# Kernel tuning notes

Measured on AMD Instinct MI355X. Metric: run time of the kernel, lower is better.

## Reference

```python
import jax, jax.numpy as jnp
import numpy as np

N = 100000   # nodes
E = 3200000  # edges (avg degree 32)
F = 128      # num_features
H = 256      # hidden_dim
D = 256      # embedding_dim
O = 2        # output_dim
BN_EPS = 1e-5


def _mk_layer(keys, fin, fmid, fout):
    kW1, kW2 = keys
    W1 = jax.random.normal(kW1, (fin, fmid), jnp.float32) / np.sqrt(fin)
    b1 = jnp.zeros((fmid,), jnp.float32)
    g = jnp.ones((fmid,), jnp.float32)
    be = jnp.zeros((fmid,), jnp.float32)
    mu = jnp.zeros((fmid,), jnp.float32)
    var = jnp.ones((fmid,), jnp.float32)
    W2 = jax.random.normal(kW2, (fmid, fout), jnp.float32) / np.sqrt(fmid)
    b2 = jnp.zeros((fout,), jnp.float32)
    return W1, b1, g, be, mu, var, W2, b2


def setup_inputs() -> dict:
    key = jax.random.key(0)
    ks = jax.random.split(key, 10)
    inp = {}
    inp["x"] = jax.random.normal(ks[0], (N, F), jnp.float32)
    inp["edge_index"] = jax.random.randint(ks[1], (2, E), 0, N, jnp.int32)
    names = ["W1", "b1", "g", "be", "mu", "var", "W2", "b2"]
    for pref, (fin, fmid, fout), kk in [
        ("l1", (F, H, H), (ks[2], ks[3])),
        ("l2", (H, H, H), (ks[4], ks[5])),
        ("l3", (H, H, D), (ks[6], ks[7])),
    ]:
        vals = _mk_layer(kk, fin, fmid, fout)
        for n, v in zip(names, vals):
            inp[f"{pref}_{n}"] = v
    inp["out_W"] = jax.random.normal(ks[8], (D, O), jnp.float32) / np.sqrt(D)
    inp["out_b"] = jnp.zeros((O,), jnp.float32)
    return inp


def gin_layer(h, src, dst, W1, b1, g, be, mu, var, W2, b2, final_relu):
    # GINConv (eps=0): z_i = x_i + sum_{j->i} x_j, then MLP(Linear-BN-ReLU-Linear[-ReLU])
    agg = jax.ops.segment_sum(h[src], dst, num_segments=N)
    z = h + agg
    z = z @ W1 + b1
    z = (z - mu) * jax.lax.rsqrt(var + BN_EPS) * g + be  # BatchNorm1d (inference)
    z = jax.nn.relu(z)
    z = z @ W2 + b2
    if final_relu:
        z = jax.nn.relu(z)
    return z


def reference(x, edge_index,
              l1_W1, l1_b1, l1_g, l1_be, l1_mu, l1_var, l1_W2, l1_b2,
              l2_W1, l2_b1, l2_g, l2_be, l2_mu, l2_var, l2_W2, l2_b2,
              l3_W1, l3_b1, l3_g, l3_be, l3_mu, l3_var, l3_W2, l3_b2,
              out_W, out_b):
    src, dst = edge_index[0], edge_index[1]
    h = gin_layer(x, src, dst, l1_W1, l1_b1, l1_g, l1_be, l1_mu, l1_var, l1_W2, l1_b2, True)
    h = gin_layer(h, src, dst, l2_W1, l2_b1, l2_g, l2_be, l2_mu, l2_var, l2_W2, l2_b2, True)
    h = gin_layer(h, src, dst, l3_W1, l3_b1, l3_g, l3_be, l3_mu, l3_var, l3_W2, l3_b2, False)
    return h @ out_W + out_b  # [N, O]
```

## Files before the change

kernel.cpp:

```cpp
#include <hip/hip_runtime.h>
#include <cstdint>
#include <cstddef>

#define N_NODES 100000
#define N_EDGES 3200000
#define MPAD    100096
#define HID     256
#define NBUCK   196
#define BSH     9
#define BSTRIDE 18432

typedef _Float16 f16;
typedef _Float16 f16x2 __attribute__((ext_vector_type(2)));
typedef _Float16 f16x8 __attribute__((ext_vector_type(8)));
typedef float    f32x4 __attribute__((ext_vector_type(4)));
typedef float    f32x2 __attribute__((ext_vector_type(2)));
typedef long long i64;

union F16x2 { unsigned u; f16 h[2]; f16x2 v; };
__device__ inline unsigned pack2(float a, float b) {
    F16x2 x; x.h[0] = (f16)a; x.h[1] = (f16)b; return x.u;
}
__device__ inline void unpack2(unsigned u, float& a, float& b) {
    F16x2 x; x.u = u; a = (float)x.h[0]; b = (float)x.h[1];
}

__global__ __launch_bounds__(256) void k_bucketA(const int* __restrict__ src,
                                                 const int* __restrict__ dst,
                                                 unsigned* __restrict__ pairs,
                                                 int* __restrict__ nb, int e) {
    __shared__ int hist[NBUCK];
    __shared__ int lbase[NBUCK];
    __shared__ int lcur[NBUCK];
    const int t = threadIdx.x;
    for (int i = t; i < NBUCK; i += 256) hist[i] = 0;
    __syncthreads();
    const int e0 = blockIdx.x * 4096;
    bool v[16]; int d[16], s[16];
#pragma unroll
    for (int i = 0; i < 16; ++i) {
        int idx = e0 + i * 256 + t;
        v[i] = idx < e;
        d[i] = v[i] ? dst[idx] : 0;
        s[i] = v[i] ? src[idx] : 0;
    }
#pragma unroll
    for (int i = 0; i < 16; ++i)
        if (v[i]) atomicAdd(&hist[d[i] >> BSH], 1);
    __syncthreads();
    for (int i = t; i < NBUCK; i += 256) {
        int h = hist[i];
        lbase[i] = h ? atomicAdd(&nb[i], h) : 0;
        lcur[i] = 0;
    }
    __syncthreads();
#pragma unroll
    for (int i = 0; i < 16; ++i) {
        if (v[i]) {
            int b = d[i] >> BSH;
            int p = atomicAdd(&lcur[b], 1);
            unsigned packed = ((unsigned)(d[i] & 511) << 17) | (unsigned)s[i];
            pairs[(size_t)b * BSTRIDE + lbase[b] + p] = packed;
        }
    }
}

__global__ void k_scan196(const int* __restrict__ nb, int* __restrict__ bbase,
                          int* __restrict__ rowptrN) {
    __shared__ int s[256];
    int t = threadIdx.x;
    int v = (t < NBUCK) ? nb[t] : 0;
    s[t] = v;
    __syncthreads();
    for (int off = 1; off < 256; off <<= 1) {
        int u = (t >= off) ? s[t - off] : 0;
        __syncthreads();
        s[t] += u;
        __syncthreads();
    }
    if (t < NBUCK) bbase[t] = s[t] - v;
    if (t == 0) *rowptrN = N_EDGES;
}

__global__ __launch_bounds__(256) void k_bucketB(const unsigned* __restrict__ pairs,
                                                 const int* __restrict__ nb,
                                                 const int* __restrict__ bbase,
                                                 int* __restrict__ rowptr,
                                                 int* __restrict__ colidx) {
    __shared__ int deg[512];
    __shared__ int sc[512];
    __shared__ int cur[512];
    const int b = blockIdx.x, t = threadIdx.x;
    const int cnt = nb[b], base = bbase[b];
    const unsigned* P = pairs + (size_t)b * BSTRIDE;
    deg[t] = 0; deg[t + 256] = 0;
    __syncthreads();
    for (int i = t; i < cnt; i += 256) atomicAdd(&deg[P[i] >> 17], 1);
    __syncthreads();
    sc[t] = deg[t]; sc[t + 256] = deg[t + 256];
    __syncthreads();
    for (int off = 1; off < 512; off <<= 1) {
        int a0 = (t >= off) ? sc[t - off] : 0;
        int a1 = (t + 256 >= off) ? sc[t + 256 - off] : 0;
        __syncthreads();
        sc[t] += a0; sc[t + 256] += a1;
        __syncthreads();
    }
    int node0 = b << BSH;
#pragma unroll
    for (int rep = 0; rep < 2; ++rep) {
        int i = t + rep * 256;
        int excl = base + sc[i] - deg[i];
        cur[i] = excl;
        int node = node0 + i;
        if (node < N_NODES) rowptr[node] = excl;
    }
    __syncthreads();
    for (int i = t; i < cnt; i += 256) {
        unsigned p = P[i];
        int pos = atomicAdd(&cur[p >> 17], 1);
        colidx[pos] = (int)(p & 0x1FFFF) << 6;
    }
}

__global__ void k_cvt8(const float2* __restrict__ x, unsigned short* __restrict__ o, int n) {
    int t = blockIdx.x * 256 + threadIdx.x;
    if (t < n) {
        float2 v = x[t];
        int pk = __builtin_amdgcn_cvt_pk_fp8_f32(v.x, v.y, 0, false);
        o[t] = (unsigned short)(pk & 0xffff);
    }
}

__global__ void k_foldw1(const float* __restrict__ W, const float* __restrict__ b1,
                         const float* __restrict__ gm, const float* __restrict__ bt,
                         const float* __restrict__ mu, const float* __restrict__ vr,
                         f16* __restrict__ Wt, float* __restrict__ bias, int K) {
    int t = blockIdx.x * 256 + threadIdx.x;
    if (t >= K * 256) return;
    int n = t & 255, k = t >> 8;
    float sc = gm[n] * rsqrtf(vr[n] + 1e-5f);
    Wt[n * K + k] = (f16)(W[t] * sc);
    if (k == 0) bias[n] = (b1[n] - mu[n]) * sc + bt[n];
}

__global__ void k_transb8(const float* __restrict__ W, unsigned char* __restrict__ W8) {
    int t = blockIdx.x * 256 + threadIdx.x;
    int n = t & 255, k = t >> 8;
    float v = W[t];
    int pk = __builtin_amdgcn_cvt_pk_fp8_f32(v, v, 0, false);
    W8[n * 256 + k] = (unsigned char)(pk & 0xff);
}

__global__ void k_fold2(const float* __restrict__ W2, const float* __restrict__ b2,
                        const float* __restrict__ outW, const float* __restrict__ outb,
                        float* __restrict__ W2o, float* __restrict__ bo) {
    int k = threadIdx.x;
    float a0 = 0.f, a1 = 0.f;
    for (int j = 0; j < 256; ++j) {
        float w = W2[k * 256 + j];
        a0 += w * outW[j * 2 + 0];
        a1 += w * outW[j * 2 + 1];
    }
    W2o[k * 2 + 0] = a0;
    W2o[k * 2 + 1] = a1;
    if (k < 2) {
        float b = outb[k];
        for (int j = 0; j < 256; ++j) b += b2[j] * outW[j * 2 + k];
        bo[k] = b;
    }
}

__global__ void k_agg256(const unsigned* __restrict__ h8,
                         const int* __restrict__ rp, const int* __restrict__ ci,
                         uint2* __restrict__ z, int n) {
    int gw = (blockIdx.x * 256 + threadIdx.x) >> 6;
    if (gw >= n) return;
    int lane = threadIdx.x & 63;
    const unsigned* h8l = h8 + lane;
    f32x2 A01, A23;
    {
        unsigned u = h8l[(size_t)gw * 64];
        A01 = __builtin_amdgcn_cvt_pk_f32_fp8(u, false);
        A23 = __builtin_amdgcn_cvt_pk_f32_fp8(u, true);
    }
    int s = rp[gw], e = rp[gw + 1];
    int p = s;
    for (; p + 7 < e; p += 8) {
        int j0 = ci[p],     j1 = ci[p + 1], j2 = ci[p + 2], j3 = ci[p + 3];
        int j4 = ci[p + 4], j5 = ci[p + 5], j6 = ci[p + 6], j7 = ci[p + 7];
        unsigned u0 = h8l[(size_t)j0], u1 = h8l[(size_t)j1];
        unsigned u2 = h8l[(size_t)j2], u3 = h8l[(size_t)j3];
        unsigned u4 = h8l[(size_t)j4], u5 = h8l[(size_t)j5];
        unsigned u6 = h8l[(size_t)j6], u7 = h8l[(size_t)j7];
#pragma unroll
        for (int q = 0; q < 8; ++q) {
            unsigned u = q == 0 ? u0 : q == 1 ? u1 : q == 2 ? u2 : q == 3 ? u3
                       : q == 4 ? u4 : q == 5 ? u5 : q == 6 ? u6 : u7;
            A01 += __builtin_amdgcn_cvt_pk_f32_fp8(u, false);
            A23 += __builtin_amdgcn_cvt_pk_f32_fp8(u, true);
        }
    }
    for (; p < e; ++p) {
        unsigned u = h8l[(size_t)ci[p]];
        A01 += __builtin_amdgcn_cvt_pk_f32_fp8(u, false);
        A23 += __builtin_amdgcn_cvt_pk_f32_fp8(u, true);
    }
    uint2 o; o.x = pack2(A01[0], A01[1]); o.y = pack2(A23[0], A23[1]);
    z[(size_t)gw * 64 + lane] = o;
}

__global__ void k_agg128(const unsigned short* __restrict__ x8,
                         const int* __restrict__ rp, const int* __restrict__ ci,
                         unsigned* __restrict__ z, int n) {
    int gw = (blockIdx.x * 256 + threadIdx.x) >> 6;
    if (gw >= n) return;
    int lane = threadIdx.x & 63;
    const unsigned short* xl = x8 + lane;
    f32x2 A01 = __builtin_amdgcn_cvt_pk_f32_fp8((unsigned)xl[(size_t)gw * 64], false);
    int s = rp[gw], e = rp[gw + 1];
    int p = s;
    for (; p + 7 < e; p += 8) {
        int j0 = ci[p],     j1 = ci[p + 1], j2 = ci[p + 2], j3 = ci[p + 3];
        int j4 = ci[p + 4], j5 = ci[p + 5], j6 = ci[p + 6], j7 = ci[p + 7];
        unsigned u0 = xl[(size_t)j0], u1 = xl[(size_t)j1];
        unsigned u2 = xl[(size_t)j2], u3 = xl[(size_t)j3];
        unsigned u4 = xl[(size_t)j4], u5 = xl[(size_t)j5];
        unsigned u6 = xl[(size_t)j6], u7 = xl[(size_t)j7];
        A01 += __builtin_amdgcn_cvt_pk_f32_fp8(u0, false);
        A01 += __builtin_amdgcn_cvt_pk_f32_fp8(u1, false);
        A01 += __builtin_amdgcn_cvt_pk_f32_fp8(u2, false);
        A01 += __builtin_amdgcn_cvt_pk_f32_fp8(u3, false);
        A01 += __builtin_amdgcn_cvt_pk_f32_fp8(u4, false);
        A01 += __builtin_amdgcn_cvt_pk_f32_fp8(u5, false);
        A01 += __builtin_amdgcn_cvt_pk_f32_fp8(u6, false);
        A01 += __builtin_amdgcn_cvt_pk_f32_fp8(u7, false);
    }
    for (; p < e; ++p)
        A01 += __builtin_amdgcn_cvt_pk_f32_fp8((unsigned)xl[(size_t)ci[p]], false);
    z[(size_t)gw * 64 + lane] = pack2(A01[0], A01[1]);
}

template <int K>
__global__ __launch_bounds__(256, 2) void k_layer(const f16* __restrict__ A,
                                                  const f16* __restrict__ W1,
                                                  const float* __restrict__ b1,
                                                  const unsigned char* __restrict__ W28,
                                                  const float* __restrict__ b2,
                                                  unsigned char* __restrict__ H8) {
    __shared__ f16 As[128 * 64];
    __shared__ f16 Bs[256 * 64];
    __shared__ unsigned char Ys[128 * 256];
    const int tid = threadIdx.x;
    const int bm0 = blockIdx.x * 128;
    const int lane = tid & 63, wave = tid >> 6;
    const int quad = lane >> 4, l16 = lane & 15;
    const int wr = (wave >> 1) * 64;
    const int wc = (wave & 1) * 128;
    const f16* Abase = A + (size_t)bm0 * K;

    {
        f32x4 acc[4][8] = {};
        for (int k0 = 0; k0 < K; k0 += 64) {
#pragma unroll
            for (int i = 0; i < 4; ++i) {
                int c = i * 256 + tid;
                int m = c >> 3;
                int gg = (c & 7) ^ (m & 7);
                __builtin_amdgcn_global_load_lds(
                    (const __attribute__((address_space(1))) unsigned int*)(Abase + (size_t)m * K + k0 + gg * 8),
                    (__attribute__((address_space(3))) unsigned int*)(As + (size_t)c * 8), 16, 0, 0);
            }
#pragma unroll
            for (int i = 0; i < 8; ++i) {
                int c = i * 256 + tid;
                int m = c >> 3;
                int gg = (c & 7) ^ (m & 7);
                __builtin_amdgcn_global_load_lds(
                    (const __attribute__((address_space(1))) unsigned int*)(W1 + (size_t)m * K + k0 + gg * 8),
                    (__attribute__((address_space(3))) unsigned int*)(Bs + (size_t)c * 8), 16, 0, 0);
            }
            __syncthreads();
#pragma unroll
            for (int kk = 0; kk < 64; kk += 32) {
                const int gbase = kk >> 3;
                f16x8 af[4], bfv[8];
#pragma unroll
                for (int mi = 0; mi < 4; ++mi) {
                    int m = wr + mi * 16 + l16;
                    int slot = (gbase + quad) ^ (m & 7);
                    af[mi] = *(const f16x8*)&As[(m * 8 + slot) * 8];
                }
#pragma unroll
                for (int ni = 0; ni < 8; ++ni) {
                    int m = wc + ni * 16 + l16;
                    int slot = (gbase + quad) ^ (m & 7);
                    bfv[ni] = *(const f16x8*)&Bs[(m * 8 + slot) * 8];
                }
#pragma unroll
                for (int mi = 0; mi < 4; ++mi)
#pragma unroll
                    for (int ni = 0; ni < 8; ++ni)
                        acc[mi][ni] = __builtin_amdgcn_mfma_f32_16x16x32_f16(af[mi], bfv[ni], acc[mi][ni], 0, 0, 0);
            }
            __syncthreads();
        }
        float bv[8];
#pragma unroll
        for (int ni = 0; ni < 8; ++ni) bv[ni] = b1[wc + ni * 16 + l16];
#pragma unroll
        for (int mi = 0; mi < 4; ++mi) {
#pragma unroll
            for (int r = 0; r < 4; ++r) {
                int row = wr + mi * 16 + quad * 4 + r;
#pragma unroll
                for (int ni = 0; ni < 8; ++ni) {
                    float v = fmaxf(acc[mi][ni][r] + bv[ni], 0.f);
                    int col = wc + ni * 16 + l16;
                    int pk = __builtin_amdgcn_cvt_pk_fp8_f32(v, v, 0, false);
                    int g = col >> 3, j = col & 7;
                    Ys[row * 256 + ((g ^ (row & 15)) * 8 + j)] = (unsigned char)(pk & 0xff);
                }
            }
        }
    }
    __syncthreads();

    unsigned char* B8 = (unsigned char*)As;
    f32x4 acc2[4][8] = {};
    for (int k0 = 0; k0 < 256; k0 += 64) {
#pragma unroll
        for (int i = 0; i < 4; ++i) {
            int c = i * 256 + tid;
            int n = c >> 2;
            int cg = c & 3;
            int gg = cg ^ (n & 3);
            __builtin_amdgcn_global_load_lds(
                (const __attribute__((address_space(1))) unsigned int*)(W28 + (size_t)n * 256 + k0 + gg * 16),
                (__attribute__((address_space(3))) unsigned int*)(B8 + (size_t)c * 16), 16, 0, 0);
        }
        __syncthreads();
#pragma unroll
        for (int kk = 0; kk < 64; kk += 32) {
            int gq = (kk >> 3) + quad;
            int gglob = ((k0 + kk) >> 3) + quad;
            i64 af[4], bf[8];
#pragma unroll
            for (int mi = 0; mi < 4; ++mi) {
                int m = wr + mi * 16 + l16;
                af[mi] = *(const i64*)&Ys[m * 256 + ((gglob ^ (m & 15)) * 8)];
            }
#pragma unroll
            for (int ni = 0; ni < 8; ++ni) {
                int n = wc + ni * 16 + l16;
                int cg2 = gq >> 1, sub = gq & 1;
                bf[ni] = *(const i64*)&B8[n * 64 + (cg2 ^ (n & 3)) * 16 + sub * 8];
            }
#pragma unroll
            for (int mi = 0; mi < 4; ++mi)
#pragma unroll
                for (int ni = 0; ni < 8; ++ni)
                    acc2[mi][ni] = __builtin_amdgcn_mfma_f32_16x16x32_fp8_fp8(af[mi], bf[ni], acc2[mi][ni], 0, 0, 0);
        }
        __syncthreads();
    }
    float bv2[8];
#pragma unroll
    for (int ni = 0; ni < 8; ++ni) bv2[ni] = b2[wc + ni * 16 + l16];
#pragma unroll
    for (int mi = 0; mi < 4; ++mi) {
#pragma unroll
        for (int r = 0; r < 4; ++r) {
            size_t row = (size_t)(bm0 + wr + mi * 16 + quad * 4 + r);
#pragma unroll
            for (int ni = 0; ni < 8; ++ni) {
                float v = fmaxf(acc2[mi][ni][r] + bv2[ni], 0.f);
                int col = wc + ni * 16 + l16;
                int pk = __builtin_amdgcn_cvt_pk_fp8_f32(v, v, 0, false);
                H8[row * HID + col] = (unsigned char)(pk & 0xff);
            }
        }
    }
}

__global__ __launch_bounds__(256, 2) void k_layer3(const f16* __restrict__ A,
                                                   const f16* __restrict__ W1,
                                                   const float* __restrict__ b1,
                                                   const float* __restrict__ W2o,
                                                   const float* __restrict__ bo,
                                                   float* __restrict__ out) {
    __shared__ f16 As[128 * 64];
    __shared__ f16 Bs[256 * 64];
    __shared__ float W2s[512];
    __shared__ float ob[256];
    const int tid = threadIdx.x;
    const int bm0 = blockIdx.x * 128;
    const int lane = tid & 63, wave = tid >> 6;
    const int quad = lane >> 4, l16 = lane & 15;
    const int wr = (wave >> 1) * 64;
    const int wc = (wave & 1) * 128;
    const f16* Abase = A + (size_t)bm0 * 256;
    W2s[tid] = W2o[tid];
    W2s[tid + 256] = W2o[tid + 256];
    ob[tid] = 0.f;

    f32x4 acc[4][8] = {};
    for (int k0 = 0; k0 < 256; k0 += 64) {
#pragma unroll
        for (int i = 0; i < 4; ++i) {
            int c = i * 256 + tid;
            int m = c >> 3;
            int gg = (c & 7) ^ (m & 7);
            __builtin_amdgcn_global_load_lds(
                (const __attribute__((address_space(1))) unsigned int*)(Abase + (size_t)m * 256 + k0 + gg * 8),
                (__attribute__((address_space(3))) unsigned int*)(As + (size_t)c * 8), 16, 0, 0);
        }
#pragma unroll
        for (int i = 0; i < 8; ++i) {
            int c = i * 256 + tid;
            int m = c >> 3;
            int gg = (c & 7) ^ (m & 7);
            __builtin_amdgcn_global_load_lds(
                (const __attribute__((address_space(1))) unsigned int*)(W1 + (size_t)m * 256 + k0 + gg * 8),
                (__attribute__((address_space(3))) unsigned int*)(Bs + (size_t)c * 8), 16, 0, 0);
        }
        __syncthreads();
#pragma unroll
        for (int kk = 0; kk < 64; kk += 32) {
            const int gbase = kk >> 3;
            f16x8 af[4], bfv[8];
#pragma unroll
            for (int mi = 0; mi < 4; ++mi) {
                int m = wr + mi * 16 + l16;
                int slot = (gbase + quad) ^ (m & 7);
                af[mi] = *(const f16x8*)&As[(m * 8 + slot) * 8];
            }
#pragma unroll
            for (int ni = 0; ni < 8; ++ni) {
                int m = wc + ni * 16 + l16;
                int slot = (gbase + quad) ^ (m & 7);
                bfv[ni] = *(const f16x8*)&Bs[(m * 8 + slot) * 8];
            }
#pragma unroll
            for (int mi = 0; mi < 4; ++mi)
#pragma unroll
                for (int ni = 0; ni < 8; ++ni)
                    acc[mi][ni] = __builtin_amdgcn_mfma_f32_16x16x32_f16(af[mi], bfv[ni], acc[mi][ni], 0, 0, 0);
        }
        __syncthreads();
    }
    float bv[8];
#pragma unroll
    for (int ni = 0; ni < 8; ++ni) bv[ni] = b1[wc + ni * 16 + l16];
#pragma unroll
    for (int mi = 0; mi < 4; ++mi) {
#pragma unroll
        for (int r = 0; r < 4; ++r) {
            int row = wr + mi * 16 + quad * 4 + r;
            float p0 = 0.f, p1 = 0.f;
#pragma unroll
            for (int ni = 0; ni < 8; ++ni) {
                float v = fmaxf(acc[mi][ni][r] + bv[ni], 0.f);
                int col = wc + ni * 16 + l16;
                p0 += v * W2s[col * 2 + 0];
                p1 += v * W2s[col * 2 + 1];
            }
#pragma unroll
            for (int off = 1; off <= 8; off <<= 1) {
                p0 += __shfl_xor(p0, off);
                p1 += __shfl_xor(p1, off);
            }
            if (l16 == 0) {
                atomicAdd(&ob[row * 2 + 0], p0);
                atomicAdd(&ob[row * 2 + 1], p1);
            }
        }
    }
    __syncthreads();
    int row = tid >> 1, o = tid & 1;
    if (bm0 + row < N_NODES)
        out[(size_t)(bm0 + row) * 2 + o] = ob[tid] + bo[o];
}

extern "C" void kernel_launch(void* const* d_in, const int* in_sizes, int n_in,
                              void* d_out, int out_size, void* d_ws, size_t ws_size,
                              hipStream_t stream) {
    const float* x    = (const float*)d_in[0];
    const int*   ei   = (const int*)d_in[1];
    const int*   esrc = ei;
    const int*   edst = ei + N_EDGES;
    const float* lw[3][8];
    for (int l = 0; l < 3; ++l)
        for (int j = 0; j < 8; ++j) lw[l][j] = (const float*)d_in[2 + l * 8 + j];
    const float* outW = (const float*)d_in[26];
    const float* outB = (const float*)d_in[27];

    char* base = (char*)d_ws;
    size_t off = 0;
    auto alloc = [&](size_t bytes) -> void* {
        void* r = base + off;
        off += (bytes + 255) & ~(size_t)255;
        return r;
    };
    f16* z  = (f16*)alloc((size_t)MPAD * 256 * 2);
    unsigned char* h8 = (unsigned char*)alloc((size_t)MPAD * 256);
    unsigned short* x8 = (unsigned short*)alloc((size_t)MPAD * 64 * 2);
    f16* W1t[3]; float* bias1[3]; unsigned char* W28[2];
    W1t[0] = (f16*)alloc(256 * 128 * 2);
    W1t[1] = (f16*)alloc(256 * 256 * 2);
    W1t[2] = (f16*)alloc(256 * 256 * 2);
    for (int l = 0; l < 2; ++l) W28[l] = (unsigned char*)alloc(256 * 256);
    for (int l = 0; l < 3; ++l) bias1[l] = (float*)alloc(256 * 4);
    float* W2o = (float*)alloc(512 * 4);
    float* bo  = (float*)alloc(2 * 4);
    unsigned* pairs = (unsigned*)alloc((size_t)NBUCK * BSTRIDE * 4);
    int* nb     = (int*)alloc(NBUCK * 4);
    int* bbase  = (int*)alloc(NBUCK * 4);
    int* rowptr = (int*)alloc((size_t)(N_NODES + 1) * 4);
    int* colidx = (int*)alloc((size_t)N_EDGES * 4);

    hipMemsetAsync(nb, 0, NBUCK * 4, stream);
    k_bucketA<<<(N_EDGES + 4095) / 4096, 256, 0, stream>>>(esrc, edst, pairs, nb, N_EDGES);
    k_scan196<<<1, 256, 0, stream>>>(nb, bbase, rowptr + N_NODES);
    k_bucketB<<<NBUCK, 256, 0, stream>>>(pairs, nb, bbase, rowptr, colidx);

    k_cvt8<<<(N_NODES * 64 + 255) / 256, 256, 0, stream>>>((const float2*)x, x8, N_NODES * 64);
    k_foldw1<<<128, 256, 0, stream>>>(lw[0][0], lw[0][1], lw[0][2], lw[0][3], lw[0][4], lw[0][5], W1t[0], bias1[0], 128);
    k_foldw1<<<256, 256, 0, stream>>>(lw[1][0], lw[1][1], lw[1][2], lw[1][3], lw[1][4], lw[1][5], W1t[1], bias1[1], 256);
    k_foldw1<<<256, 256, 0, stream>>>(lw[2][0], lw[2][1], lw[2][2], lw[2][3], lw[2][4], lw[2][5], W1t[2], bias1[2], 256);
    k_transb8<<<256, 256, 0, stream>>>(lw[0][6], W28[0]);
    k_transb8<<<256, 256, 0, stream>>>(lw[1][6], W28[1]);
    k_fold2<<<1, 256, 0, stream>>>(lw[2][6], lw[2][7], outW, outB, W2o, bo);

    const int GG = MPAD / 128;
    const int WBLOCKS = (N_NODES + 3) / 4;

    k_agg128<<<WBLOCKS, 256, 0, stream>>>(x8, rowptr, colidx, (unsigned*)z, N_NODES);
    k_layer<128><<<GG, 256, 0, stream>>>(z, W1t[0], bias1[0], W28[0], lw[0][7], h8);
    k_agg256<<<WBLOCKS, 256, 0, stream>>>((const unsigned*)h8, rowptr, colidx, (uint2*)z, N_NODES);
    k_layer<256><<<GG, 256, 0, stream>>>(z, W1t[1], bias1[1], W28[1], lw[1][7], h8);
    k_agg256<<<WBLOCKS, 256, 0, stream>>>((const unsigned*)h8, rowptr, colidx, (uint2*)z, N_NODES);
    k_layer3<<<GG, 256, 0, stream>>>(z, W1t[2], bias1[2], W2o, bo, (float*)d_out);
}
```

Baseline: 686.4 us.

## Alias LDS buffers and split B fragments to fit three blocks per CU

The separate Bs and Ys shared arrays in k_layer become one 32KB aliased buffer, cutting LDS per block so three blocks can be resident. Launch bounds rise to 3 blocks per SM for k_layer and k_layer3, and the B-fragment loads are split into two halves of four to lower register pressure. The intermediate FP8 activations are scaled by 1/8, with the W2 FP8 weights and the aggregation outputs scaled by 8 to compensate. This keeps values in FP8 range after the reuse, but it changes rounding behaviour, and the tighter register budget may cause spills.

```diff
diff --git a/kernel.cpp b/kernel.cpp
--- a/kernel.cpp
+++ b/kernel.cpp
@@ -20,9 +20,6 @@
 union F16x2 { unsigned u; f16 h[2]; f16x2 v; };
 __device__ inline unsigned pack2(float a, float b) {
     F16x2 x; x.h[0] = (f16)a; x.h[1] = (f16)b; return x.u;
-}
-__device__ inline void unpack2(unsigned u, float& a, float& b) {
-    F16x2 x; x.u = u; a = (float)x.h[0]; b = (float)x.h[1];
 }
 
 __global__ __launch_bounds__(256) void k_bucketA(const int* __restrict__ src,
@@ -147,7 +144,7 @@
 __global__ void k_transb8(const float* __restrict__ W, unsigned char* __restrict__ W8) {
     int t = blockIdx.x * 256 + threadIdx.x;
     int n = t & 255, k = t >> 8;
-    float v = W[t];
+    float v = W[t] * 8.f;
     int pk = __builtin_amdgcn_cvt_pk_fp8_f32(v, v, 0, false);
     W8[n * 256 + k] = (unsigned char)(pk & 0xff);
 }
@@ -206,7 +203,9 @@
         A01 += __builtin_amdgcn_cvt_pk_f32_fp8(u, false);
         A23 += __builtin_amdgcn_cvt_pk_f32_fp8(u, true);
     }
-    uint2 o; o.x = pack2(A01[0], A01[1]); o.y = pack2(A23[0], A23[1]);
+    uint2 o;
+    o.x = pack2(A01[0] * 8.f, A01[1] * 8.f);
+    o.y = pack2(A23[0] * 8.f, A23[1] * 8.f);
     z[(size_t)gw * 64 + lane] = o;
 }
 
@@ -242,15 +241,16 @@
 }
 
 template <int K>
-__global__ __launch_bounds__(256, 2) void k_layer(const f16* __restrict__ A,
+__global__ __launch_bounds__(256, 3) void k_layer(const f16* __restrict__ A,
                                                   const f16* __restrict__ W1,
                                                   const float* __restrict__ b1,
                                                   const unsigned char* __restrict__ W28,
                                                   const float* __restrict__ b2,
                                                   unsigned char* __restrict__ H8) {
     __shared__ f16 As[128 * 64];
-    __shared__ f16 Bs[256 * 64];
-    __shared__ unsigned char Ys[128 * 256];
+    __shared__ __align__(16) char BsYs[32 * 1024];
+    f16* Bs = (f16*)BsYs;
+    unsigned char* Ys = (unsigned char*)BsYs;
     const int tid = threadIdx.x;
     const int bm0 = blockIdx.x * 128;
     const int lane = tid & 63, wave = tid >> 6;
@@ -259,52 +259,56 @@
     const int wc = (wave & 1) * 128;
     const f16* Abase = A + (size_t)bm0 * K;
 
+    f32x4 acc[4][8] = {};
+    for (int k0 = 0; k0 < K; k0 += 64) {
+#pragma unroll
+        for (int i = 0; i < 4; ++i) {
+            int c = i * 256 + tid;
+            int m = c >> 3;
+            int gg = (c & 7) ^ (m & 7);
+            __builtin_amdgcn_global_load_lds(
+                (const __attribute__((address_space(1))) unsigned int*)(Abase + (size_t)m * K + k0 + gg * 8),
+                (__attribute__((address_space(3))) unsigned int*)(As + (size_t)c * 8), 16, 0, 0);
+        }
+#pragma unroll
+        for (int i = 0; i < 8; ++i) {
+            int c = i * 256 + tid;
+            int m = c >> 3;
+            int gg = (c & 7) ^ (m & 7);
+            __builtin_amdgcn_global_load_lds(
+                (const __attribute__((address_space(1))) unsigned int*)(W1 + (size_t)m * K + k0 + gg * 8),
+                (__attribute__((address_space(3))) unsigned int*)(Bs + (size_t)c * 8), 16, 0, 0);
+        }
+        __syncthreads();
+#pragma unroll
+        for (int kk = 0; kk < 64; kk += 32) {
+            const int gbase = kk >> 3;
+            f16x8 af[4];
+#pragma unroll
+            for (int mi = 0; mi < 4; ++mi) {
+                int m = wr + mi * 16 + l16;
+                int slot = (gbase + quad) ^ (m & 7);
+                af[mi] = *(const f16x8*)&As[(m * 8 + slot) * 8];
+            }
+#pragma unroll
+            for (int hh = 0; hh < 2; ++hh) {
+                f16x8 bfv[4];
+#pragma unroll
+                for (int nj = 0; nj < 4; ++nj) {
+                    int m = wc + (hh * 4 + nj) * 16 + l16;
+                    int slot = (gbase + quad) ^ (m & 7);
+                    bfv[nj] = *(const f16x8*)&Bs[(m * 8 + slot) * 8];
+                }
+#pragma unroll
+                for (int mi = 0; mi < 4; ++mi)
+#pragma unroll
+                    for (int nj = 0; nj < 4; ++nj)
+                        acc[mi][hh * 4 + nj] = __builtin_amdgcn_mfma_f32_16x16x32_f16(af[mi], bfv[nj], acc[mi][hh * 4 + nj], 0, 0, 0);
+            }
+        }
+        __syncthreads();
+    }
     {
-        f32x4 acc[4][8] = {};
-        for (int k0 = 0; k0 < K; k0 += 64) {
-#pragma unroll
-            for (int i = 0; i < 4; ++i) {
-                int c = i * 256 + tid;
-                int m = c >> 3;
-                int gg = (c & 7) ^ (m & 7);
-                __builtin_amdgcn_global_load_lds(
-                    (const __attribute__((address_space(1))) unsigned int*)(Abase + (size_t)m * K + k0 + gg * 8),
-                    (__attribute__((address_space(3))) unsigned int*)(As + (size_t)c * 8), 16, 0, 0);
-            }
-#pragma unroll
-            for (int i = 0; i < 8; ++i) {
-                int c = i * 256 + tid;
-                int m = c >> 3;
-                int gg = (c & 7) ^ (m & 7);
-                __builtin_amdgcn_global_load_lds(
-                    (const __attribute__((address_space(1))) unsigned int*)(W1 + (size_t)m * K + k0 + gg * 8),
-                    (__attribute__((address_space(3))) unsigned int*)(Bs + (size_t)c * 8), 16, 0, 0);
-            }
-            __syncthreads();
-#pragma unroll
-            for (int kk = 0; kk < 64; kk += 32) {
-                const int gbase = kk >> 3;
-                f16x8 af[4], bfv[8];
-#pragma unroll
-                for (int mi = 0; mi < 4; ++mi) {
-                    int m = wr + mi * 16 + l16;
-                    int slot = (gbase + quad) ^ (m & 7);
-                    af[mi] = *(const f16x8*)&As[(m * 8 + slot) * 8];
-                }
-#pragma unroll
-                for (int ni = 0; ni < 8; ++ni) {
-                    int m = wc + ni * 16 + l16;
-                    int slot = (gbase + quad) ^ (m & 7);
-                    bfv[ni] = *(const f16x8*)&Bs[(m * 8 + slot) * 8];
-                }
-#pragma unroll
-                for (int mi = 0; mi < 4; ++mi)
-#pragma unroll
-                    for (int ni = 0; ni < 8; ++ni)
-                        acc[mi][ni] = __builtin_amdgcn_mfma_f32_16x16x32_f16(af[mi], bfv[ni], acc[mi][ni], 0, 0, 0);
-            }
-            __syncthreads();
-        }
         float bv[8];
 #pragma unroll
         for (int ni = 0; ni < 8; ++ni) bv[ni] = b1[wc + ni * 16 + l16];
@@ -315,7 +319,7 @@
                 int row = wr + mi * 16 + quad * 4 + r;
 #pragma unroll
                 for (int ni = 0; ni < 8; ++ni) {
-                    float v = fmaxf(acc[mi][ni][r] + bv[ni], 0.f);
+                    float v = fmaxf(acc[mi][ni][r] + bv[ni], 0.f) * 0.125f;
                     int col = wc + ni * 16 + l16;
                     int pk = __builtin_amdgcn_cvt_pk_fp8_f32(v, v, 0, false);
                     int g = col >> 3, j = col & 7;
@@ -344,23 +348,27 @@
         for (int kk = 0; kk < 64; kk += 32) {
             int gq = (kk >> 3) + quad;
             int gglob = ((k0 + kk) >> 3) + quad;
-            i64 af[4], bf[8];
+            i64 af[4];
 #pragma unroll
             for (int mi = 0; mi < 4; ++mi) {
                 int m = wr + mi * 16 + l16;
                 af[mi] = *(const i64*)&Ys[m * 256 + ((gglob ^ (m & 15)) * 8)];
             }
 #pragma unroll
-            for (int ni = 0; ni < 8; ++ni) {
-                int n = wc + ni * 16 + l16;
-                int cg2 = gq >> 1, sub = gq & 1;
-                bf[ni] = *(const i64*)&B8[n * 64 + (cg2 ^ (n & 3)) * 16 + sub * 8];
-            }
-#pragma unroll
-            for (int mi = 0; mi < 4; ++mi)
-#pragma unroll
-                for (int ni = 0; ni < 8; ++ni)
-                    acc2[mi][ni] = __builtin_amdgcn_mfma_f32_16x16x32_fp8_fp8(af[mi], bf[ni], acc2[mi][ni], 0, 0, 0);
+            for (int hh = 0; hh < 2; ++hh) {
+                i64 bf[4];
+#pragma unroll
+                for (int nj = 0; nj < 4; ++nj) {
+                    int n = wc + (hh * 4 + nj) * 16 + l16;
+                    int cg2 = gq >> 1, sub = gq & 1;
+                    bf[nj] = *(const i64*)&B8[n * 64 + (cg2 ^ (n & 3)) * 16 + sub * 8];
+                }
+#pragma unroll
+                for (int mi = 0; mi < 4; ++mi)
+#pragma unroll
+                    for (int nj = 0; nj < 4; ++nj)
+                        acc2[mi][hh * 4 + nj] = __builtin_amdgcn_mfma_f32_16x16x32_fp8_fp8(af[mi], bf[nj], acc2[mi][hh * 4 + nj], 0, 0, 0);
+            }
         }
         __syncthreads();
     }
@@ -374,7 +382,7 @@
             size_t row = (size_t)(bm0 + wr + mi * 16 + quad * 4 + r);
 #pragma unroll
             for (int ni = 0; ni < 8; ++ni) {
-                float v = fmaxf(acc2[mi][ni][r] + bv2[ni], 0.f);
+                float v = fmaxf(acc2[mi][ni][r] + bv2[ni], 0.f) * 0.125f;
                 int col = wc + ni * 16 + l16;
                 int pk = __builtin_amdgcn_cvt_pk_fp8_f32(v, v, 0, false);
                 H8[row * HID + col] = (unsigned char)(pk & 0xff);
@@ -383,7 +391,7 @@
     }
 }
 
-__global__ __launch_bounds__(256, 2) void k_layer3(const f16* __restrict__ A,
+__global__ __launch_bounds__(256, 3) void k_layer3(const f16* __restrict__ A,
                                                    const f16* __restrict__ W1,
                                                    const float* __restrict__ b1,
                                                    const float* __restrict__ W2o,
@@ -428,7 +436,7 @@
 #pragma unroll
         for (int kk = 0; kk < 64; kk += 32) {
             const int gbase = kk >> 3;
-            f16x8 af[4], bfv[8];
+            f16x8 af[4];
 #pragma unroll
             for (int mi = 0; mi < 4; ++mi) {
                 int m = wr + mi * 16 + l16;
@@ -436,16 +444,20 @@
                 af[mi] = *(const f16x8*)&As[(m * 8 + slot) * 8];
             }
 #pragma unroll
-            for (int ni = 0; ni < 8; ++ni) {
-                int m = wc + ni * 16 + l16;
-                int slot = (gbase + quad) ^ (m & 7);
-                bfv[ni] = *(const f16x8*)&Bs[(m * 8 + slot) * 8];
-            }
-#pragma unroll
-            for (int mi = 0; mi < 4; ++mi)
-#pragma unroll
-                for (int ni = 0; ni < 8; ++ni)
-                    acc[mi][ni] = __builtin_amdgcn_mfma_f32_16x16x32_f16(af[mi], bfv[ni], acc[mi][ni], 0, 0, 0);
+            for (int hh = 0; hh < 2; ++hh) {
+                f16x8 bfv[4];
+#pragma unroll
+                for (int nj = 0; nj < 4; ++nj) {
+                    int m = wc + (hh * 4 + nj) * 16 + l16;
+                    int slot = (gbase + quad) ^ (m & 7);
+                    bfv[nj] = *(const f16x8*)&Bs[(m * 8 + slot) * 8];
+                }
+#pragma unroll
+                for (int mi = 0; mi < 4; ++mi)
+#pragma unroll
+                    for (int nj = 0; nj < 4; ++nj)
+                        acc[mi][hh * 4 + nj] = __builtin_amdgcn_mfma_f32_16x16x32_f16(af[mi], bfv[nj], acc[mi][hh * 4 + nj], 0, 0, 0);
+            }
         }
         __syncthreads();
     }
```

Measured after the change: 777.2 us. 13.2% more time.
